# Kernel tuning notes

Hardware: AMD Instinct MI355X
Metric: run time of the kernel (lower is better)

The kernel has to match this reference:

```python
import jax, jax.numpy as jnp
import numpy as np

D_MODEL = 1024
NUM_HEADS = 16
D_K = D_MODEL // NUM_HEADS


def setup_inputs() -> dict:
    key = jax.random.key(0)
    ks = jax.random.split(key, 11)
    B, S = 4, 2048
    s = 1.0 / np.sqrt(D_MODEL)
    return {
        "q": jax.random.normal(ks[0], (B, S, D_MODEL), jnp.float32),
        "k": jax.random.normal(ks[1], (B, S, D_MODEL), jnp.float32),
        "v": jax.random.normal(ks[2], (B, S, D_MODEL), jnp.float32),
        "WQ": jax.random.normal(ks[3], (D_MODEL, D_MODEL), jnp.float32) * s,
        "bQ": jax.random.normal(ks[4], (D_MODEL,), jnp.float32) * 0.01,
        "WK": jax.random.normal(ks[5], (D_MODEL, D_MODEL), jnp.float32) * s,
        "bK": jax.random.normal(ks[6], (D_MODEL,), jnp.float32) * 0.01,
        "WV": jax.random.normal(ks[7], (D_MODEL, D_MODEL), jnp.float32) * s,
        "bV": jax.random.normal(ks[8], (D_MODEL,), jnp.float32) * 0.01,
        "W0": jax.random.normal(ks[9], (D_MODEL, D_MODEL), jnp.float32) * s,
        "b0": jax.random.normal(ks[10], (D_MODEL,), jnp.float32) * 0.01,
    }


def reference(q, k, v, WQ, bQ, WK, bK, WV, bV, W0, b0):
    B, S, _ = q.shape
    H, Dk = NUM_HEADS, D_K

    def proj(x, W, b):
        # nn.Linear: x @ W.T + b, then split heads -> [B, H, S, Dk]
        return (x @ W.T + b).reshape(B, S, H, Dk).transpose(0, 2, 1, 3)

    Q = proj(q, WQ, bQ)
    K = proj(k, WK, bK)
    V = proj(v, WV, bV)

    # Quirk of original module: softmax on UNSCALED scores, then divide
    # by sqrt(d_k) AFTER softmax.
    score = jnp.einsum("bhqd,bhkd->bhqk", Q, K)  # [B,H,S,S]
    attn = jax.nn.softmax(score, axis=-1) / jnp.sqrt(jnp.float32(Dk))
    out = jnp.einsum("bhqk,bhkd->bhqd", attn, V)  # [B,H,S,Dk]

    out = out.transpose(0, 2, 1, 3).reshape(B, S, H * Dk)
    return out @ W0.T + b0
```

## Files before the change

### kernel.cpp

```cpp
#include <hip/hip_runtime.h>

typedef __attribute__((ext_vector_type(4))) float f32x4;
typedef __attribute__((ext_vector_type(8))) short bf16x8;
typedef __attribute__((ext_vector_type(8))) unsigned short u16x8;
typedef __attribute__((ext_vector_type(4))) unsigned short u16x4;
typedef __attribute__((ext_vector_type(4))) unsigned int u32x4;

#define DEV static __device__ __forceinline__

#define BQ 4
#define SQ 2048
#define DM 1024
#define HH 16
#define DK 64
#define MM (BQ * SQ)

DEV unsigned short f2bf(float f) {
    unsigned int u = __builtin_bit_cast(unsigned int, f);
    u += 0x7fffu + ((u >> 16) & 1u);
    return (unsigned short)(u >> 16);
}

DEV unsigned int cvtpk(float lo, float hi) {
    unsigned int r;
    asm("v_cvt_pk_bf16_f32 %0, %1, %2" : "=v"(r) : "v"(lo), "v"(hi));
    return r;
}

DEV void gll16(const void* g, void* l) {
    __builtin_amdgcn_global_load_lds(
        (const __attribute__((address_space(1))) unsigned int*)g,
        (__attribute__((address_space(3))) unsigned int*)l, 16, 0, 0);
}

#define SWZ128(b) ((b) ^ ((((b) >> 7) & 7) << 4))

DEV u16x8 pack8(const f32x4 a, const f32x4 b) {
    u32x4 d;
    d[0] = cvtpk(a[0], a[1]); d[1] = cvtpk(a[2], a[3]);
    d[2] = cvtpk(b[0], b[1]); d[3] = cvtpk(b[2], b[3]);
    return __builtin_bit_cast(u16x8, d);
}

__global__ __launch_bounds__(256)
void conv_w(const float* __restrict__ WQ, const float* __restrict__ WK,
            const float* __restrict__ WV, const float* __restrict__ W0,
            unsigned short* __restrict__ wq, unsigned short* __restrict__ wk,
            unsigned short* __restrict__ wv, unsigned short* __restrict__ w0)
{
    const unsigned int NW = 1u << 17;
    const unsigned int total = 4 * NW;
    for (unsigned int idx = blockIdx.x * 256 + threadIdx.x; idx < total;
         idx += gridDim.x * 256) {
        const unsigned int s = idx >> 17, off = idx & (NW - 1);
        const float* src = (s == 0) ? WQ : (s == 1) ? WK : (s == 2) ? WV : W0;
        unsigned short* dst = (s == 0) ? wq : (s == 1) ? wk : (s == 2) ? wv : w0;
        const f32x4 a = *(const f32x4*)(src + (size_t)off * 8);
        const f32x4 b = *(const f32x4*)(src + (size_t)off * 8 + 4);
        *(u16x8*)(dst + (size_t)off * 8) = pack8(a, b);
    }
}

__global__ __launch_bounds__(256, 3)
void gemm_qkv(const float* __restrict__ qf, const float* __restrict__ kf,
              const float* __restrict__ vf,
              const unsigned short* __restrict__ wq,
              const unsigned short* __restrict__ wk,
              const unsigned short* __restrict__ wv,
              const float* __restrict__ bQ, const float* __restrict__ bK,
              const float* __restrict__ bV,
              unsigned short* __restrict__ Qb, unsigned short* __restrict__ Kb,
              unsigned short* __restrict__ Vtb)
{
    __shared__ char Asb[16384];
    __shared__ char Bsb[16384];

    const int z = blockIdx.z;
    const float* A32        = (z == 0) ? qf : (z == 1) ? kf : vf;
    const unsigned short* W = (z == 0) ? wq : (z == 1) ? wk : wv;
    const float* bias       = (z == 0) ? bQ : (z == 1) ? bK : bV;
    unsigned short* C       = (z == 0) ? Qb : (z == 1) ? Kb : Vtb;

    const int tid = threadIdx.x, lane = tid & 63, wid = tid >> 6;
    const int l15 = lane & 15, lg = lane >> 4;
    const int wr = wid >> 1, wc = wid & 1;
    const int m0 = blockIdx.x * 128, n0 = blockIdx.y * 128;

    const int sg  = tid & 7;
    const int sr0 = tid >> 3;
    const int swz = sg ^ (sr0 & 7);

    f32x4 acc[4][4];
#pragma unroll
    for (int i = 0; i < 4; ++i)
#pragma unroll
        for (int j = 0; j < 4; ++j) acc[i][j] = (f32x4){0.f, 0.f, 0.f, 0.f};

    f32x4 anx[4][2];
#pragma unroll
    for (int j = 0; j < 4; ++j) {
        const float* p = A32 + (size_t)(m0 + j * 32 + sr0) * DM + sg * 8;
        anx[j][0] = *(const f32x4*)p;
        anx[j][1] = *(const f32x4*)(p + 4);
    }

    for (int kt = 0; kt < 16; ++kt) {
        __syncthreads();
#pragma unroll
        for (int j = 0; j < 4; ++j) {
            const int r = j * 32 + sr0;
            u32x4 d;
            d[0] = cvtpk(anx[j][0][0], anx[j][0][1]);
            d[1] = cvtpk(anx[j][0][2], anx[j][0][3]);
            d[2] = cvtpk(anx[j][1][0], anx[j][1][1]);
            d[3] = cvtpk(anx[j][1][2], anx[j][1][3]);
            *(u32x4*)(Asb + r * 128 + swz * 16) = d;
        }
#pragma unroll
        for (int i_ = 0; i_ < 4; ++i_) {
            const int r_ = i_ * 32 + wid * 8 + (lane >> 3);
            const int g_ = (lane & 7) ^ (r_ & 7);
            gll16(W + (size_t)(n0 + r_) * 1024 + kt * 64 + g_ * 8,
                  Bsb + i_ * 4096 + wid * 1024);
        }
        __syncthreads();
        if (kt < 15) {
#pragma unroll
            for (int j = 0; j < 4; ++j) {
                const float* p = A32 + (size_t)(m0 + j * 32 + sr0) * DM +
                                 (kt + 1) * 64 + sg * 8;
                anx[j][0] = *(const f32x4*)p;
                anx[j][1] = *(const f32x4*)(p + 4);
            }
        }
#pragma unroll
        for (int ki = 0; ki < 2; ++ki) {
            bf16x8 af[4], bw[4];
#pragma unroll
            for (int mi = 0; mi < 4; ++mi) {
                const int r = wr * 64 + mi * 16 + l15;
                const int p = (ki * 4 + lg) ^ (r & 7);
                af[mi] = *(const bf16x8*)(Asb + r * 128 + p * 16);
            }
#pragma unroll
            for (int ni = 0; ni < 4; ++ni) {
                const int r = wc * 64 + ni * 16 + l15;
                const int p = (ki * 4 + lg) ^ (r & 7);
                bw[ni] = *(const bf16x8*)(Bsb + r * 128 + p * 16);
            }
#pragma unroll
            for (int mi = 0; mi < 4; ++mi)
#pragma unroll
                for (int ni = 0; ni < 4; ++ni)
                    acc[mi][ni] = __builtin_amdgcn_mfma_f32_16x16x32_bf16(
                        af[mi], bw[ni], acc[mi][ni], 0, 0, 0);
        }
    }

#pragma unroll
    for (int ni = 0; ni < 4; ++ni) {
        const int n = n0 + wc * 64 + ni * 16 + l15;
        const float bb = bias[n];
        const int h = n >> 6, d = n & 63;
#pragma unroll
        for (int mi = 0; mi < 4; ++mi) {
            const int mbase = m0 + wr * 64 + mi * 16 + lg * 4;
            if (z != 2) {
#pragma unroll
                for (int j = 0; j < 4; ++j) {
                    const int m = mbase + j, b = m >> 11, s = m & 2047;
                    C[(((size_t)(b * HH + h)) * SQ + s) * DK + d] =
                        f2bf(acc[mi][ni][j] + bb);
                }
            } else {
                u16x4 pk;
#pragma unroll
                for (int j = 0; j < 4; ++j) pk[j] = f2bf(acc[mi][ni][j] + bb);
                const int m = mbase, b = m >> 11, s = m & 2047;
                const int sp = (s & ~31) | (((s >> 2) & 3) << 3) | (((s >> 4) & 1) << 2);
                *(u16x4*)&C[(((size_t)(b * HH + h)) * DK + d) * SQ + sp] = pk;
            }
        }
    }
}

__global__ __launch_bounds__(256, 3)
void gemm_out(const unsigned short* __restrict__ Av,
              const unsigned short* __restrict__ Wv,
              const float* __restrict__ bias, float* __restrict__ Cv)
{
    __shared__ char Asb[16384];
    __shared__ char Bsb[16384];

    const int tid = threadIdx.x, lane = tid & 63, wid = tid >> 6;
    const int l15 = lane & 15, lg = lane >> 4;
    const int wr = wid >> 1, wc = wid & 1;
    const int m0 = blockIdx.x * 128, n0 = blockIdx.y * 128;

    f32x4 acc[4][4];
#pragma unroll
    for (int i = 0; i < 4; ++i)
#pragma unroll
        for (int j = 0; j < 4; ++j) acc[i][j] = (f32x4){0.f, 0.f, 0.f, 0.f};

    for (int kt = 0; kt < 16; ++kt) {
        __syncthreads();
#pragma unroll
        for (int i_ = 0; i_ < 4; ++i_) {
            const int r_ = i_ * 32 + wid * 8 + (lane >> 3);
            const int g_ = (lane & 7) ^ (r_ & 7);
            gll16(Av + (size_t)(m0 + r_) * 1024 + kt * 64 + g_ * 8,
                  Asb + i_ * 4096 + wid * 1024);
            gll16(Wv + (size_t)(n0 + r_) * 1024 + kt * 64 + g_ * 8,
                  Bsb + i_ * 4096 + wid * 1024);
        }
        __syncthreads();
#pragma unroll
        for (int ki = 0; ki < 2; ++ki) {
            bf16x8 af[4], bw[4];
#pragma unroll
            for (int mi = 0; mi < 4; ++mi) {
                const int r = wr * 64 + mi * 16 + l15;
                const int p = (ki * 4 + lg) ^ (r & 7);
                af[mi] = *(const bf16x8*)(Asb + r * 128 + p * 16);
            }
#pragma unroll
            for (int ni = 0; ni < 4; ++ni) {
                const int r = wc * 64 + ni * 16 + l15;
                const int p = (ki * 4 + lg) ^ (r & 7);
                bw[ni] = *(const bf16x8*)(Bsb + r * 128 + p * 16);
            }
#pragma unroll
            for (int mi = 0; mi < 4; ++mi)
#pragma unroll
                for (int ni = 0; ni < 4; ++ni)
                    acc[mi][ni] = __builtin_amdgcn_mfma_f32_16x16x32_bf16(
                        af[mi], bw[ni], acc[mi][ni], 0, 0, 0);
        }
    }

#pragma unroll
    for (int ni = 0; ni < 4; ++ni) {
        const int n = n0 + wc * 64 + ni * 16 + l15;
        const float bb = bias[n];
#pragma unroll
        for (int mi = 0; mi < 4; ++mi) {
            const int mbase = m0 + wr * 64 + mi * 16 + lg * 4;
#pragma unroll
            for (int j = 0; j < 4; ++j)
                Cv[(size_t)(mbase + j) * DM + n] = acc[mi][ni][j] + bb;
        }
    }
}

__global__ __launch_bounds__(256, 4)
void flash_attn(const unsigned short* __restrict__ Qb,
                const unsigned short* __restrict__ Kb,
                const unsigned short* __restrict__ Vtb,
                unsigned short* __restrict__ outA)
{
    __shared__ unsigned short Ks[2][64 * 64];
    __shared__ unsigned short Vs[2][64 * 64];

    const int tid = threadIdx.x, lane = tid & 63, wid = tid >> 6;
    const int l15 = lane & 15, lg = lane >> 4;

    const int flat = blockIdx.x + (blockIdx.y << 4);
    const int xcd = flat & 7;
    const int qblk = (flat >> 3) & 15;
    const int bh = ((flat >> 7) << 3) + xcd;
    const int q0 = qblk * 128;

    const unsigned short* Qp = Qb + (size_t)bh * SQ * DK;
    const unsigned short* Kp = Kb + (size_t)bh * SQ * DK;
    const unsigned short* Vp = Vtb + (size_t)bh * DK * SQ;

    bf16x8 qf[2][2];
#pragma unroll
    for (int mi = 0; mi < 2; ++mi)
#pragma unroll
        for (int ki = 0; ki < 2; ++ki)
            qf[mi][ki] = *(const bf16x8*)&Qp[(size_t)(q0 + wid * 32 + mi * 16 + l15) * DK +
                                             ki * 32 + lg * 8];

    f32x4 O[2][4];
    f32x4 lsum[2];
#pragma unroll
    for (int mi = 0; mi < 2; ++mi) {
        lsum[mi] = (f32x4){0.f, 0.f, 0.f, 0.f};
#pragma unroll
        for (int di = 0; di < 4; ++di) O[mi][di] = (f32x4){0.f, 0.f, 0.f, 0.f};
    }

    const float L2E = 1.44269504089f;
    const float NC  = -92.33248261689366f;

#define STAGE(BUF, KV0) do {                                                   \
        char* Ksb_ = (char*)Ks[BUF]; char* Vsb_ = (char*)Vs[BUF];              \
        _Pragma("unroll")                                                      \
        for (int i_ = 0; i_ < 2; ++i_) {                                       \
            const int p_ = (wid * 2 + i_) * 1024 + lane * 16;                  \
            gll16((const char*)Kp + (size_t)(KV0) * 128 + SWZ128(p_),          \
                  Ksb_ + (wid * 2 + i_) * 1024);                               \
            const int d_ = p_ >> 7;                                            \
            const int cb_ = (p_ ^ ((d_ & 7) << 4)) & 127;                      \
            gll16((const char*)Vp + (size_t)d_ * 4096 + (KV0) * 2 + cb_,       \
                  Vsb_ + (wid * 2 + i_) * 1024);                               \
        } } while (0)

    STAGE(0, 0);
    asm volatile("s_waitcnt vmcnt(0)" ::: "memory");
    __syncthreads();

    for (int kt = 0; kt < 32; ++kt) {
        const int cur = kt & 1;
        const char* Ksb = (const char*)Ks[cur];
        const char* Vsb = (const char*)Vs[cur];
        if (kt < 31) STAGE(cur ^ 1, (kt + 1) * 64);

        f32x4 Sf[2][4];
#pragma unroll
        for (int mi = 0; mi < 2; ++mi)
#pragma unroll
            for (int ni = 0; ni < 4; ++ni) Sf[mi][ni] = (f32x4){0.f, 0.f, 0.f, 0.f};
        __builtin_amdgcn_s_setprio(1);
#pragma unroll
        for (int ki = 0; ki < 2; ++ki) {
#pragma unroll
            for (int ni = 0; ni < 4; ++ni) {
                const int o = (ni * 16 + l15) * 128 + ki * 64 + lg * 16;
                const bf16x8 kf2 = *(const bf16x8*)(Ksb + SWZ128(o));
                Sf[0][ni] = __builtin_amdgcn_mfma_f32_16x16x32_bf16(kf2, qf[0][ki], Sf[0][ni], 0, 0, 0);
                Sf[1][ni] = __builtin_amdgcn_mfma_f32_16x16x32_bf16(kf2, qf[1][ki], Sf[1][ni], 0, 0, 0);
            }
        }
        __builtin_amdgcn_s_setprio(0);

#pragma unroll
        for (int mi = 0; mi < 2; ++mi) {
#pragma unroll
            for (int ni = 0; ni < 4; ++ni) {
#pragma unroll
                for (int j = 0; j < 4; ++j)
                    Sf[mi][ni][j] = __builtin_amdgcn_exp2f(
                        __builtin_fmaf(Sf[mi][ni][j], L2E, NC));
                lsum[mi] += Sf[mi][ni];
            }
        }

#pragma unroll
        for (int kk = 0; kk < 2; ++kk) {
            bf16x8 pf[2];
#pragma unroll
            for (int mi = 0; mi < 2; ++mi) {
                u32x4 pd;
                pd[0] = cvtpk(Sf[mi][2 * kk][0],     Sf[mi][2 * kk][1]);
                pd[1] = cvtpk(Sf[mi][2 * kk][2],     Sf[mi][2 * kk][3]);
                pd[2] = cvtpk(Sf[mi][2 * kk + 1][0], Sf[mi][2 * kk + 1][1]);
                pd[3] = cvtpk(Sf[mi][2 * kk + 1][2], Sf[mi][2 * kk + 1][3]);
                pf[mi] = __builtin_bit_cast(bf16x8, pd);
            }
            __builtin_amdgcn_s_setprio(1);
#pragma unroll
            for (int di = 0; di < 4; ++di) {
                const int o = (di * 16 + l15) * 128 + kk * 64 + lg * 16;
                const bf16x8 vf2 = *(const bf16x8*)(Vsb + SWZ128(o));
                O[0][di] = __builtin_amdgcn_mfma_f32_16x16x32_bf16(vf2, pf[0], O[0][di], 0, 0, 0);
                O[1][di] = __builtin_amdgcn_mfma_f32_16x16x32_bf16(vf2, pf[1], O[1][di], 0, 0, 0);
            }
            __builtin_amdgcn_s_setprio(0);
        }

        asm volatile("s_waitcnt vmcnt(0)" ::: "memory");
        __syncthreads();
    }

    const int b = bh >> 4, h = bh & 15;
#pragma unroll
    for (int mi = 0; mi < 2; ++mi) {
        const f32x4 l4 = lsum[mi];
        float lt = (l4[0] + l4[1]) + (l4[2] + l4[3]);
        lt += __shfl_xor(lt, 16);
        lt += __shfl_xor(lt, 32);
        const float inv = 1.f / (8.f * lt);
        const int q = q0 + wid * 32 + mi * 16 + l15;
#pragma unroll
        for (int di = 0; di < 4; ++di) {
            u16x4 pk;
#pragma unroll
            for (int j = 0; j < 4; ++j) pk[j] = f2bf(O[mi][di][j] * inv);
            *(u16x4*)&outA[((size_t)(b * SQ + q)) * DM + h * DK + di * 16 + lg * 4] = pk;
        }
    }
#undef STAGE
}

extern "C" void kernel_launch(void* const* d_in, const int* in_sizes, int n_in,
                              void* d_out, int out_size, void* d_ws, size_t ws_size,
                              hipStream_t stream)
{
    (void)in_sizes; (void)n_in; (void)out_size; (void)ws_size;
    const float* q  = (const float*)d_in[0];
    const float* k  = (const float*)d_in[1];
    const float* v  = (const float*)d_in[2];
    const float* WQ = (const float*)d_in[3];
    const float* bQ = (const float*)d_in[4];
    const float* WK = (const float*)d_in[5];
    const float* bK = (const float*)d_in[6];
    const float* WV = (const float*)d_in[7];
    const float* bV = (const float*)d_in[8];
    const float* W0 = (const float*)d_in[9];
    const float* b0 = (const float*)d_in[10];

    unsigned short* ws = (unsigned short*)d_ws;
    const size_t NEL = (size_t)MM * DM;
    const size_t NW  = (size_t)DM * DM;
    unsigned short* Qb  = ws;
    unsigned short* Kb  = ws + NEL;
    unsigned short* Vtb = ws + 2 * NEL;
    unsigned short* Ab  = ws + 3 * NEL;
    unsigned short* wq  = ws + 4 * NEL;
    unsigned short* wk  = wq + NW;
    unsigned short* wv  = wk + NW;
    unsigned short* w0  = wv + NW;

    dim3 blk(256);
    hipLaunchKernelGGL(conv_w, dim3(512), blk, 0, stream,
                       WQ, WK, WV, W0, wq, wk, wv, w0);
    hipLaunchKernelGGL(gemm_qkv, dim3(MM / 128, DM / 128, 3), blk, 0, stream,
                       q, k, v, wq, wk, wv, bQ, bK, bV, Qb, Kb, Vtb);
    hipLaunchKernelGGL(flash_attn, dim3(SQ / 128, BQ * HH), blk, 0, stream,
                       Qb, Kb, Vtb, Ab);
    hipLaunchKernelGGL(gemm_out, dim3(MM / 128, DM / 128), blk, 0, stream,
                       Ab, w0, b0, (float*)d_out);
}
```

Baseline: 193.7 us.

## Double-buffer weight tiles and prefetch A two steps ahead in QKV GEMM

Restructures the QKV projection GEMM main loop into a software pipeline. The weight tile for the next k-step goes into a second LDS buffer, and the fp32 A tile is prefetched two steps ahead into alternating register sets. A manual s_waitcnt vmcnt(24) plus s_barrier replaces one __syncthreads so loads can stay in flight across the MFMA compute. The cost is 16KB more LDS and extra registers, which may lower occupancy under launch_bounds(256,3). The hand-tuned vmcnt count risks being wrong, and the final steps issue redundant wrapped loads.

```diff
diff --git a/kernel.cpp b/kernel.cpp
--- a/kernel.cpp
+++ b/kernel.cpp
@@ -73,7 +73,8 @@
               unsigned short* __restrict__ Vtb)
 {
     __shared__ char Asb[16384];
-    __shared__ char Bsb[16384];
+    __shared__ char Bsb0[16384];
+    __shared__ char Bsb1[16384];
 
     const int z = blockIdx.z;
     const float* A32        = (z == 0) ? qf : (z == 1) ? kf : vf;
@@ -96,66 +97,79 @@
 #pragma unroll
         for (int j = 0; j < 4; ++j) acc[i][j] = (f32x4){0.f, 0.f, 0.f, 0.f};
 
-    f32x4 anx[4][2];
-#pragma unroll
-    for (int j = 0; j < 4; ++j) {
-        const float* p = A32 + (size_t)(m0 + j * 32 + sr0) * DM + sg * 8;
-        anx[j][0] = *(const f32x4*)p;
-        anx[j][1] = *(const f32x4*)(p + 4);
-    }
-
-    for (int kt = 0; kt < 16; ++kt) {
-        __syncthreads();
-#pragma unroll
-        for (int j = 0; j < 4; ++j) {
-            const int r = j * 32 + sr0;
-            u32x4 d;
-            d[0] = cvtpk(anx[j][0][0], anx[j][0][1]);
-            d[1] = cvtpk(anx[j][0][2], anx[j][0][3]);
-            d[2] = cvtpk(anx[j][1][0], anx[j][1][1]);
-            d[3] = cvtpk(anx[j][1][2], anx[j][1][3]);
-            *(u32x4*)(Asb + r * 128 + swz * 16) = d;
-        }
-#pragma unroll
-        for (int i_ = 0; i_ < 4; ++i_) {
-            const int r_ = i_ * 32 + wid * 8 + (lane >> 3);
-            const int g_ = (lane & 7) ^ (r_ & 7);
-            gll16(W + (size_t)(n0 + r_) * 1024 + kt * 64 + g_ * 8,
-                  Bsb + i_ * 4096 + wid * 1024);
-        }
-        __syncthreads();
-        if (kt < 15) {
-#pragma unroll
-            for (int j = 0; j < 4; ++j) {
-                const float* p = A32 + (size_t)(m0 + j * 32 + sr0) * DM +
-                                 (kt + 1) * 64 + sg * 8;
-                anx[j][0] = *(const f32x4*)p;
-                anx[j][1] = *(const f32x4*)(p + 4);
-            }
-        }
-#pragma unroll
-        for (int ki = 0; ki < 2; ++ki) {
-            bf16x8 af[4], bw[4];
-#pragma unroll
-            for (int mi = 0; mi < 4; ++mi) {
-                const int r = wr * 64 + mi * 16 + l15;
-                const int p = (ki * 4 + lg) ^ (r & 7);
-                af[mi] = *(const bf16x8*)(Asb + r * 128 + p * 16);
-            }
-#pragma unroll
-            for (int ni = 0; ni < 4; ++ni) {
-                const int r = wc * 64 + ni * 16 + l15;
-                const int p = (ki * 4 + lg) ^ (r & 7);
-                bw[ni] = *(const bf16x8*)(Bsb + r * 128 + p * 16);
-            }
-#pragma unroll
-            for (int mi = 0; mi < 4; ++mi)
-#pragma unroll
-                for (int ni = 0; ni < 4; ++ni)
-                    acc[mi][ni] = __builtin_amdgcn_mfma_f32_16x16x32_bf16(
-                        af[mi], bw[ni], acc[mi][ni], 0, 0, 0);
-        }
-    }
+    f32x4 aA[4][2], aB[4][2];
+
+#define LOAD_A(AREG, KT) do {                                                  \
+        const int kta_ = (KT) & 15;                                            \
+        _Pragma("unroll")                                                      \
+        for (int j = 0; j < 4; ++j) {                                          \
+            const float* p = A32 + (size_t)(m0 + j * 32 + sr0) * DM +          \
+                             kta_ * 64 + sg * 8;                               \
+            AREG[j][0] = *(const f32x4*)p;                                     \
+            AREG[j][1] = *(const f32x4*)(p + 4);                               \
+        } } while (0)
+
+#define ISSUE_W(BUFP, KT) do {                                                 \
+        const int ktw_ = (KT) & 15;                                            \
+        _Pragma("unroll")                                                      \
+        for (int i_ = 0; i_ < 4; ++i_) {                                       \
+            const int r_ = i_ * 32 + wid * 8 + (lane >> 3);                    \
+            const int g_ = (lane & 7) ^ (r_ & 7);                              \
+            gll16(W + (size_t)(n0 + r_) * 1024 + ktw_ * 64 + g_ * 8,           \
+                  (BUFP) + i_ * 4096 + wid * 1024);                            \
+        } } while (0)
+
+#define QKV_STEP(KT, AREG, BCUR, BNXT)                                         \
+    {   asm volatile("s_barrier" ::: "memory");           \
+        _Pragma("unroll")                                                      \
+        for (int j = 0; j < 4; ++j) {                      \
+            const int r = j * 32 + sr0;                                        \
+            u32x4 d;                                                           \
+            d[0] = cvtpk(AREG[j][0][0], AREG[j][0][1]);                        \
+            d[1] = cvtpk(AREG[j][0][2], AREG[j][0][3]);                        \
+            d[2] = cvtpk(AREG[j][1][0], AREG[j][1][1]);                        \
+            d[3] = cvtpk(AREG[j][1][2], AREG[j][1][3]);                        \
+            *(u32x4*)(Asb + r * 128 + swz * 16) = d;                           \
+        }                                                                      \
+        ISSUE_W(BNXT, (KT) + 1);                            \
+        LOAD_A(AREG, (KT) + 2);                             \
+        asm volatile("s_waitcnt vmcnt(24) lgkmcnt(0)\n\ts_barrier"             \
+                     ::: "memory");                          \
+        _Pragma("unroll")                                                      \
+        for (int ki = 0; ki < 2; ++ki) {                                       \
+            bf16x8 af[4], bw[4];                                               \
+            _Pragma("unroll")                                                  \
+            for (int mi = 0; mi < 4; ++mi) {                                   \
+                const int r = wr * 64 + mi * 16 + l15;                         \
+                const int p = (ki * 4 + lg) ^ (r & 7);                         \
+                af[mi] = *(const bf16x8*)(Asb + r * 128 + p * 16);             \
+            }                                                                  \
+            _Pragma("unroll")                                                  \
+            for (int ni = 0; ni < 4; ++ni) {                                   \
+                const int r = wc * 64 + ni * 16 + l15;                         \
+                const int p = (ki * 4 + lg) ^ (r & 7);                         \
+                bw[ni] = *(const bf16x8*)((BCUR) + r * 128 + p * 16);          \
+            }                                                                  \
+            _Pragma("unroll")                                                  \
+            for (int mi = 0; mi < 4; ++mi)                                     \
+                _Pragma("unroll")                                              \
+                for (int ni = 0; ni < 4; ++ni)                                 \
+                    acc[mi][ni] = __builtin_amdgcn_mfma_f32_16x16x32_bf16(     \
+                        af[mi], bw[ni], acc[mi][ni], 0, 0, 0);                 \
+        }                                                                      \
+    }
+
+    LOAD_A(aA, 0);
+    ISSUE_W(Bsb0, 0);
+    LOAD_A(aB, 1);
+
+    for (int kt2 = 0; kt2 < 16; kt2 += 2) {
+        QKV_STEP(kt2,     aA, Bsb0, Bsb1)
+        QKV_STEP(kt2 + 1, aB, Bsb1, Bsb0)
+    }
+#undef QKV_STEP
+#undef ISSUE_W
+#undef LOAD_A
 
 #pragma unroll
     for (int ni = 0; ni < 4; ++ni) {
```

Result: slower. 431.1 us (median of 2 runs) (+122.5%).
